# Performance work log

Hardware: AMD Instinct MI355X
Metric: run time of the kernel (lower is better)

Reference implementation:

```python
import jax, jax.numpy as jnp
import numpy as np

VOCAB = 40000
U = 128  # num_trans_units


def setup_inputs() -> dict:
    key = jax.random.key(0)
    ks = jax.random.split(key, 10)
    B, S, T, L = 16, 512, 64, 64
    sents = jax.random.randint(ks[0], (B, S), 0, 30000)
    triples = jax.random.randint(ks[1], (B, T, L, 3), 0, VOCAB)
    sent_triples = jax.random.randint(ks[2], (B, S, 1), 0, T)
    scale = 0.05
    emb_table = jax.random.normal(ks[3], (VOCAB, U), jnp.float32)
    W_trans = jax.random.normal(ks[4], (U, U), jnp.float32) * scale
    b_trans = jnp.zeros((U,), jnp.float32)
    W_ht = jax.random.normal(ks[5], (2 * U, U), jnp.float32) * scale
    b_ht = jnp.zeros((U,), jnp.float32)
    W_rel = jax.random.normal(ks[6], (U, U), jnp.float32) * scale
    b_rel = jnp.zeros((U,), jnp.float32)
    return {
        "sents": sents, "triples": triples, "sent_triples": sent_triples,
        "emb_table": emb_table,
        "W_trans": W_trans, "b_trans": b_trans,
        "W_ht": W_ht, "b_ht": b_ht,
        "W_rel": W_rel, "b_rel": b_rel,
    }


def reference(sents, triples, sent_triples, emb_table,
              W_trans, b_trans, W_ht, b_ht, W_rel, b_rel):
    # triples: [B, T, L, 3] int ids -> embed [B, T, L, 3, U]
    emb = emb_table[triples]
    # fc_trans_transform: Linear(U,U) + Tanh on last dim
    te = jnp.tanh(emb @ W_trans + b_trans)            # [B,T,L,3,U]
    head, relation, tail = te[..., 0, :], te[..., 1, :], te[..., 2, :]
    head_tail = jnp.concatenate([head, tail], axis=-1)  # [B,T,L,2U]
    ht_t = jnp.tanh(head_tail @ W_ht + b_ht)             # [B,T,L,U]
    rel_t = relation @ W_rel + b_rel                     # [B,T,L,U]
    e_weight = jnp.sum(rel_t * ht_t, axis=-1)            # [B,T,L]
    alpha = jax.nn.softmax(e_weight, axis=-1)            # over triple_len L
    graph_embed = jnp.sum(alpha[..., None] * head_tail, axis=2)  # [B,T,2U]
    # gather_nd: out[b, s] = graph_embed[b, sent_triples[b, s, 0]]
    idx = sent_triples[..., 0]                           # [B,S]
    out = jnp.take_along_axis(graph_embed, idx[:, :, None], axis=1)  # [B,S,2U]
    return out
```

## Files before the change

kernel.cpp:

```cpp
#include <hip/hip_runtime.h>
#include <cstdint>
#include <cstddef>

typedef short short8 __attribute__((ext_vector_type(8)));
typedef float f32x4 __attribute__((ext_vector_type(4)));

#define BB 16
#define SS 512
#define TT 64
#define LL 64
#define UU 128

#define WT_OFF    0u
#define WHT_OFF   (WT_OFF + 32768u)
#define WREL_OFF  (WHT_OFF + 65536u)
#define EMBBF_OFF (WREL_OFF + 32768u)
#define EMBBF_BYTES (40000u * 128u * 2u)

__device__ __forceinline__ unsigned short f2bf(float x) {
  unsigned u = __float_as_uint(x);
  unsigned r = ((u >> 16) & 1u) + 0x7FFFu;
  return (unsigned short)((u + r) >> 16);
}
__device__ __forceinline__ float bf2f(unsigned short h) {
  return __uint_as_float(((unsigned)h) << 16);
}
__device__ __forceinline__ float ftanh(float x) {
  float e = __expf(2.0f * x);
  return 1.0f - __fdividef(2.0f, e + 1.0f);
}
__device__ __forceinline__ unsigned cvtpk(float a, float b) {
  unsigned r;
  asm("v_cvt_pk_bf16_f32 %0, %1, %2" : "=v"(r) : "v"(a), "v"(b));
  return r;
}

__global__ void prep_kernel(const float* __restrict__ Wt,
                            const float* __restrict__ Wht,
                            const float* __restrict__ Wrel,
                            const float* __restrict__ ef,
                            unsigned char* __restrict__ ws) {
  int blk = blockIdx.x;
  if (blk < 32) {
    int slot = blk * 256 + threadIdx.x;
    const float* W;
    unsigned char* base;
    if (slot < 2048)      { W = Wt;   base = ws + WT_OFF; }
    else if (slot < 6144) { W = Wht;  base = ws + WHT_OFF;  slot -= 2048; }
    else                  { W = Wrel; base = ws + WREL_OFF; slot -= 6144; }
    int lane = slot & 63, pair = slot >> 6;
    int n  = (pair & 7) * 16 + (lane & 15);
    int k0 = (pair >> 3) * 32 + (lane >> 4) * 8;
    short8 hv;
    #pragma unroll
    for (int j = 0; j < 8; ++j)
      hv[j] = (short)f2bf(W[(size_t)(k0 + j) * UU + n]);
    *reinterpret_cast<short8*>(base + (size_t)pair * 1024 + lane * 16) = hv;
  } else {
    int i = (blk - 32) * 256 + threadIdx.x;
    const float4 a = reinterpret_cast<const float4*>(ef)[i * 2];
    const float4 b = reinterpret_cast<const float4*>(ef)[i * 2 + 1];
    short8 v;
    v[0] = (short)f2bf(a.x); v[1] = (short)f2bf(a.y);
    v[2] = (short)f2bf(a.z); v[3] = (short)f2bf(a.w);
    v[4] = (short)f2bf(b.x); v[5] = (short)f2bf(b.y);
    v[6] = (short)f2bf(b.z); v[7] = (short)f2bf(b.w);
    reinterpret_cast<short8*>(ws + EMBBF_OFF)[i] = v;
  }
}

template<bool PRE>
__launch_bounds__(1024, 8)
__global__ void fused_bt(const int* __restrict__ triples,
                         const float* __restrict__ emb_f32,
                         const unsigned short* __restrict__ emb_bf,
                         const float* __restrict__ b_trans,
                         const float* __restrict__ b_ht,
                         const float* __restrict__ b_rel,
                         const int* __restrict__ sent_triples,
                         const unsigned char* __restrict__ wsr,
                         float* __restrict__ out) {
  __shared__ unsigned short TEB[192 * 128];
  __shared__ float EWt[8][64];
  __shared__ float ALPHA[64];
  __shared__ float PART[4][256];
  int* TOKs = reinterpret_cast<int*>(&PART[0][0]);

  const int tid  = threadIdx.x;
  const int bt   = blockIdx.x;
  const int w    = tid >> 6;
  const int lane = tid & 63;
  const int li   = lane & 15;
  const int lg   = lane >> 4;
  const int nt   = w & 7;
  const int rh   = w >> 3;

  if (tid < 48)
    reinterpret_cast<int4*>(TOKs)[tid] =
        reinterpret_cast<const int4*>(triples + (size_t)bt * 192)[tid];

  const unsigned char* wtb  = wsr + WT_OFF;
  const unsigned char* whtb = wsr + WHT_OFF;
  const unsigned char* wrlb = wsr + WREL_OFF;
  const float bhv   = b_ht[nt * 16 + li];
  const float brlv  = b_rel[nt * 16 + li];
  const float4 btr4 = *reinterpret_cast<const float4*>(b_trans + nt * 16 + lg * 4);
  __syncthreads();

  {
    short8 st[3];
    #pragma unroll
    for (int j = 0; j < 3; ++j) {
      int o = tid + j * 1024;
      int row = o >> 4, pc = o & 15;
      int clog = pc ^ (row & 15);
      if (PRE) {
        st[j] = *reinterpret_cast<const short8*>(
            emb_bf + (size_t)TOKs[row] * UU + clog * 8);
      } else {
        const float* fb = emb_f32 + (size_t)TOKs[row] * UU + clog * 8;
        float4 x = *reinterpret_cast<const float4*>(fb);
        float4 y = *reinterpret_cast<const float4*>(fb + 4);
        st[j][0]=(short)f2bf(x.x); st[j][1]=(short)f2bf(x.y);
        st[j][2]=(short)f2bf(x.z); st[j][3]=(short)f2bf(x.w);
        st[j][4]=(short)f2bf(y.x); st[j][5]=(short)f2bf(y.y);
        st[j][6]=(short)f2bf(y.z); st[j][7]=(short)f2bf(y.w);
      }
    }
    #pragma unroll
    for (int j = 0; j < 3; ++j) {
      int o = tid + j * 1024;
      int row = o >> 4, pc = o & 15;
      *reinterpret_cast<short8*>(&TEB[row * 128 + pc * 8]) = st[j];
    }
  }

  short8 B1h[4];
  #pragma unroll
  for (int kt = 0; kt < 4; ++kt)
    B1h[kt] = *reinterpret_cast<const short8*>(
        wtb + (size_t)(kt * 8 + nt) * 1024 + lane * 16);
  __syncthreads();

  const int cc8 = nt * 2 + (lg >> 1);
  const int hb8 = (lg & 1) << 3;

  f32x4 acc[6];
  #pragma unroll
  for (int q = 0; q < 6; ++q) acc[q] = f32x4{0.f, 0.f, 0.f, 0.f};

  #pragma unroll
  for (int kt = 0; kt < 4; ++kt) {
    #pragma unroll
    for (int q = 0; q < 6; ++q) {
      const short8 b = *reinterpret_cast<const short8*>(
          &TEB[((rh * 6 + q) * 16 + li) * 128 + (((kt * 4 + lg) ^ li) << 3)]);
      acc[q] = __builtin_amdgcn_mfma_f32_16x16x32_bf16(B1h[kt], b, acc[q], 0, 0, 0);
    }
  }
  __syncthreads();

  #pragma unroll
  for (int q = 0; q < 6; ++q) {
    int row = (rh * 6 + q) * 16 + li;
    float v0 = ftanh(acc[q][0] + btr4.x);
    float v1 = ftanh(acc[q][1] + btr4.y);
    float v2 = ftanh(acc[q][2] + btr4.z);
    float v3 = ftanh(acc[q][3] + btr4.w);
    uint2 pk = { cvtpk(v0, v1), cvtpk(v2, v3) };
    *reinterpret_cast<uint2*>(
        reinterpret_cast<char*>(TEB) + row * 256 +
        (((cc8 ^ li) << 4) | hb8)) = pk;
  }

  short8 Wc = *reinterpret_cast<const short8*>(
      whtb + (size_t)nt * 1024 + lane * 16);
  __syncthreads();

  const int mh = rh * 2;
  f32x4 accH[2] = {{0.f,0.f,0.f,0.f},{0.f,0.f,0.f,0.f}};
  f32x4 accR[2] = {{0.f,0.f,0.f,0.f},{0.f,0.f,0.f,0.f}};

  #pragma unroll
  for (int kt = 0; kt < 8; ++kt) {
    short8 Wn;
    if (kt < 7)
      Wn = *reinterpret_cast<const short8*>(
          whtb + (size_t)((kt + 1) * 8 + nt) * 1024 + lane * 16);
    else
      Wn = *reinterpret_cast<const short8*>(
          wrlb + (size_t)nt * 1024 + lane * 16);
    const int koff = (kt < 4) ? 0 : 2;
    const int c16  = (kt & 3) * 4 + lg;
    #pragma unroll
    for (int mi = 0; mi < 2; ++mi) {
      const int row = 48 * (mh + mi) + 3 * li + koff;
      const short8 a = *reinterpret_cast<const short8*>(
          &TEB[row * 128 + ((c16 ^ (row & 15)) << 3)]);
      accH[mi] = __builtin_amdgcn_mfma_f32_16x16x32_bf16(a, Wc, accH[mi], 0, 0, 0);
    }
    Wc = Wn;
  }
  #pragma unroll
  for (int kt = 0; kt < 4; ++kt) {
    short8 Wn;
    if (kt < 3)
      Wn = *reinterpret_cast<const short8*>(
          wrlb + (size_t)((kt + 1) * 8 + nt) * 1024 + lane * 16);
    const int c16 = kt * 4 + lg;
    #pragma unroll
    for (int mi = 0; mi < 2; ++mi) {
      const int row = 48 * (mh + mi) + 3 * li + 1;
      const short8 a = *reinterpret_cast<const short8*>(
          &TEB[row * 128 + ((c16 ^ (row & 15)) << 3)]);
      accR[mi] = __builtin_amdgcn_mfma_f32_16x16x32_bf16(a, Wc, accR[mi], 0, 0, 0);
    }
    Wc = Wn;
  }

  #pragma unroll
  for (int mi = 0; mi < 2; ++mi) {
    #pragma unroll
    for (int r = 0; r < 4; ++r) {
      float p = ftanh(accH[mi][r] + bhv) * (accR[mi][r] + brlv);
      p += __shfl_xor(p, 1, 64);
      p += __shfl_xor(p, 2, 64);
      p += __shfl_xor(p, 4, 64);
      p += __shfl_xor(p, 8, 64);
      if (li == 0) EWt[nt][(mh + mi) * 16 + lg * 4 + r] = p;
    }
  }
  __syncthreads();

  if (tid < 64) {
    float e = 0.f;
    #pragma unroll
    for (int n = 0; n < 8; ++n) e += EWt[n][tid];
    float mx = e;
    #pragma unroll
    for (int off = 32; off > 0; off >>= 1)
      mx = fmaxf(mx, __shfl_xor(mx, off, 64));
    float ex = __expf(e - mx);
    float sm = ex;
    #pragma unroll
    for (int off = 32; off > 0; off >>= 1)
      sm += __shfl_xor(sm, off, 64);
    ALPHA[tid] = ex / sm;
  }
  __syncthreads();

  {
    int c = tid & 255, lgp = tid >> 8;
    int k  = (c >> 7) * 2;
    int cc = c & 127;
    int w8 = cc >> 3, b7 = cc & 7;
    float o = 0.f;
    #pragma unroll
    for (int j = 0; j < 16; ++j) {
      int l = lgp * 16 + j;
      int row = 3 * l + k;
      o = fmaf(ALPHA[l],
               bf2f(TEB[row * 128 + (((w8 ^ (row & 15)) << 3) | b7)]), o);
    }
    PART[lgp][c] = o;
  }
  __syncthreads();

  int* MATCH = reinterpret_cast<int*>(&EWt[0][0]);
  int* NM    = reinterpret_cast<int*>(&ALPHA[0]);
  if (tid < 256)
    PART[0][tid] = PART[0][tid] + PART[1][tid] + PART[2][tid] + PART[3][tid];
  if (tid == 0) *NM = 0;
  __syncthreads();

  {
    int b = bt >> 6, t = bt & 63;
    if (tid < SS) {
      int idx = sent_triples[b * SS + tid];
      if (idx == t) {
        int slot = atomicAdd(NM, 1);
        MATCH[slot] = tid;
      }
    }
    __syncthreads();
    const int nm = *NM;
    const float4 v = reinterpret_cast<const float4*>(&PART[0][0])[lane];
    for (int q = w; q < nm; q += 16) {
      int s = MATCH[q];
      reinterpret_cast<float4*>(out + ((size_t)(b * SS + s)) * 256)[lane] = v;
    }
  }
}

extern "C" void kernel_launch(void* const* d_in, const int* in_sizes, int n_in,
                              void* d_out, int out_size, void* d_ws, size_t ws_size,
                              hipStream_t stream) {
  const int*   triples      = (const int*)d_in[1];
  const int*   sent_triples = (const int*)d_in[2];
  const float* emb_table    = (const float*)d_in[3];
  const float* W_trans      = (const float*)d_in[4];
  const float* b_trans      = (const float*)d_in[5];
  const float* W_ht         = (const float*)d_in[6];
  const float* b_ht         = (const float*)d_in[7];
  const float* W_rel        = (const float*)d_in[8];
  const float* b_rel        = (const float*)d_in[9];
  float* out = (float*)d_out;
  unsigned char* ws = (unsigned char*)d_ws;
  unsigned short* emb_bf = (unsigned short*)(ws + EMBBF_OFF);

  const bool pre = ws_size >= (size_t)EMBBF_OFF + EMBBF_BYTES;

  prep_kernel<<<pre ? 2532 : 32, 256, 0, stream>>>(
      W_trans, W_ht, W_rel, emb_table, ws);

  if (pre)
    fused_bt<true><<<BB * TT, 1024, 0, stream>>>(
        triples, emb_table, emb_bf, b_trans, b_ht, b_rel, sent_triples, ws, out);
  else
    fused_bt<false><<<BB * TT, 1024, 0, stream>>>(
        triples, emb_table, emb_bf, b_trans, b_ht, b_rel, sent_triples, ws, out);
}
```

Before: 50.17 us.

## Rework wave tiling, async gather to LDS, DPP reductions, and hoist match scan

```diff
diff --git a/kernel.cpp b/kernel.cpp
--- a/kernel.cpp
+++ b/kernel.cpp
@@ -17,14 +17,20 @@
 #define EMBBF_OFF (WREL_OFF + 32768u)
 #define EMBBF_BYTES (40000u * 128u * 2u)
 
+#if defined(__has_builtin)
+#  if __has_builtin(__builtin_amdgcn_global_load_lds)
+#    define USE_GLDS 1
+#  endif
+#endif
+#ifndef USE_GLDS
+#  define USE_GLDS 0
+#endif
+
 __device__ __forceinline__ unsigned short f2bf(float x) {
   unsigned u = __float_as_uint(x);
   unsigned r = ((u >> 16) & 1u) + 0x7FFFu;
   return (unsigned short)((u + r) >> 16);
 }
-__device__ __forceinline__ float bf2f(unsigned short h) {
-  return __uint_as_float(((unsigned)h) << 16);
-}
 __device__ __forceinline__ float ftanh(float x) {
   float e = __expf(2.0f * x);
   return 1.0f - __fdividef(2.0f, e + 1.0f);
@@ -34,6 +40,20 @@
   asm("v_cvt_pk_bf16_f32 %0, %1, %2" : "=v"(r) : "v"(a), "v"(b));
   return r;
 }
+__device__ __forceinline__ float row16_sum(float x) {
+  x += __int_as_float(__builtin_amdgcn_update_dpp(0, __float_as_int(x), 0xB1, 0xF, 0xF, true));
+  x += __int_as_float(__builtin_amdgcn_update_dpp(0, __float_as_int(x), 0x4E, 0xF, 0xF, true));
+  x += __int_as_float(__builtin_amdgcn_update_dpp(0, __float_as_int(x), 0x141, 0xF, 0xF, true));
+  x += __int_as_float(__builtin_amdgcn_update_dpp(0, __float_as_int(x), 0x140, 0xF, 0xF, true));
+  return x;
+}
+#if USE_GLDS
+__device__ __forceinline__ void g2lds16(const void* g, void* l) {
+  __builtin_amdgcn_global_load_lds(
+      (const unsigned int __attribute__((address_space(1)))*)g,
+      (unsigned int __attribute__((address_space(3)))*)l, 16, 0, 0);
+}
+#endif
 
 __global__ void prep_kernel(const float* __restrict__ Wt,
                             const float* __restrict__ Wht,
@@ -81,10 +101,11 @@
                          const unsigned char* __restrict__ wsr,
                          float* __restrict__ out) {
   __shared__ unsigned short TEB[192 * 128];
-  __shared__ float EWt[8][64];
+  __shared__ float EWt[4][64];
   __shared__ float ALPHA[64];
-  __shared__ float PART[4][256];
-  int* TOKs = reinterpret_cast<int*>(&PART[0][0]);
+  __shared__ float PART[8][256];
+  __shared__ int MATCH[512];
+  __shared__ int NM;
 
   const int tid  = threadIdx.x;
   const int bt   = blockIdx.x;
@@ -92,150 +113,182 @@
   const int lane = tid & 63;
   const int li   = lane & 15;
   const int lg   = lane >> 4;
-  const int nt   = w & 7;
-  const int rh   = w >> 3;
-
-  if (tid < 48)
-    reinterpret_cast<int4*>(TOKs)[tid] =
-        reinterpret_cast<const int4*>(triples + (size_t)bt * 192)[tid];
+  const int ntp  = w & 3;
+  const int nt0  = ntp * 2, nt1 = nt0 + 1;
+  const int grp  = w >> 2;
 
   const unsigned char* wtb  = wsr + WT_OFF;
   const unsigned char* whtb = wsr + WHT_OFF;
   const unsigned char* wrlb = wsr + WREL_OFF;
-  const float bhv   = b_ht[nt * 16 + li];
-  const float brlv  = b_rel[nt * 16 + li];
-  const float4 btr4 = *reinterpret_cast<const float4*>(b_trans + nt * 16 + lg * 4);
-  __syncthreads();
-
-  {
-    short8 st[3];
+
+  if (tid == 0) NM = 0;
+
+  if (PRE) {
+#if USE_GLDS
     #pragma unroll
     for (int j = 0; j < 3; ++j) {
       int o = tid + j * 1024;
       int row = o >> 4, pc = o & 15;
-      int clog = pc ^ (row & 15);
-      if (PRE) {
-        st[j] = *reinterpret_cast<const short8*>(
-            emb_bf + (size_t)TOKs[row] * UU + clog * 8);
-      } else {
-        const float* fb = emb_f32 + (size_t)TOKs[row] * UU + clog * 8;
-        float4 x = *reinterpret_cast<const float4*>(fb);
-        float4 y = *reinterpret_cast<const float4*>(fb + 4);
-        st[j][0]=(short)f2bf(x.x); st[j][1]=(short)f2bf(x.y);
-        st[j][2]=(short)f2bf(x.z); st[j][3]=(short)f2bf(x.w);
-        st[j][4]=(short)f2bf(y.x); st[j][5]=(short)f2bf(y.y);
-        st[j][6]=(short)f2bf(y.z); st[j][7]=(short)f2bf(y.w);
-      }
+      int tok = triples[(size_t)bt * 192 + row];
+      g2lds16(emb_bf + (size_t)tok * UU + ((pc ^ (row & 15)) << 3),
+              &TEB[o * 8]);
+    }
+#else
+    short8 st[3];
+    #pragma unroll
+    for (int j = 0; j < 3; ++j) {
+      int o = tid + j * 1024, row = o >> 4, pc = o & 15;
+      int tok = triples[(size_t)bt * 192 + row];
+      st[j] = *reinterpret_cast<const short8*>(
+          emb_bf + (size_t)tok * UU + ((pc ^ (row & 15)) << 3));
     }
     #pragma unroll
     for (int j = 0; j < 3; ++j) {
       int o = tid + j * 1024;
-      int row = o >> 4, pc = o & 15;
-      *reinterpret_cast<short8*>(&TEB[row * 128 + pc * 8]) = st[j];
-    }
-  }
-
-  short8 B1h[4];
-  #pragma unroll
-  for (int kt = 0; kt < 4; ++kt)
-    B1h[kt] = *reinterpret_cast<const short8*>(
-        wtb + (size_t)(kt * 8 + nt) * 1024 + lane * 16);
-  __syncthreads();
-
-  const int cc8 = nt * 2 + (lg >> 1);
-  const int hb8 = (lg & 1) << 3;
-
-  f32x4 acc[6];
-  #pragma unroll
-  for (int q = 0; q < 6; ++q) acc[q] = f32x4{0.f, 0.f, 0.f, 0.f};
-
+      *reinterpret_cast<short8*>(&TEB[o * 8]) = st[j];
+    }
+#endif
+  } else {
+    short8 st[3];
+    #pragma unroll
+    for (int j = 0; j < 3; ++j) {
+      int o = tid + j * 1024, row = o >> 4, pc = o & 15;
+      int tok = triples[(size_t)bt * 192 + row];
+      const float* fb = emb_f32 + (size_t)tok * UU + ((pc ^ (row & 15)) << 3);
+      float4 x = *reinterpret_cast<const float4*>(fb);
+      float4 y = *reinterpret_cast<const float4*>(fb + 4);
+      st[j][0]=(short)f2bf(x.x); st[j][1]=(short)f2bf(x.y);
+      st[j][2]=(short)f2bf(x.z); st[j][3]=(short)f2bf(x.w);
+      st[j][4]=(short)f2bf(y.x); st[j][5]=(short)f2bf(y.y);
+      st[j][6]=(short)f2bf(y.z); st[j][7]=(short)f2bf(y.w);
+    }
+    #pragma unroll
+    for (int j = 0; j < 3; ++j) {
+      int o = tid + j * 1024;
+      *reinterpret_cast<short8*>(&TEB[o * 8]) = st[j];
+    }
+  }
+
+  short8 Wa = *reinterpret_cast<const short8*>(wtb + (size_t)nt0 * 1024 + lane * 16);
+  short8 Wb = *reinterpret_cast<const short8*>(wtb + (size_t)nt1 * 1024 + lane * 16);
+  __syncthreads();
+
+  if (tid < SS) {
+    int idx = sent_triples[(bt >> 6) * SS + tid];
+    if (idx == (bt & 63)) MATCH[atomicAdd(&NM, 1)] = tid;
+  }
+
+  f32x4 acc[3][2];
+  #pragma unroll
+  for (int q = 0; q < 3; ++q) {
+    acc[q][0] = f32x4{0.f, 0.f, 0.f, 0.f};
+    acc[q][1] = f32x4{0.f, 0.f, 0.f, 0.f};
+  }
   #pragma unroll
   for (int kt = 0; kt < 4; ++kt) {
-    #pragma unroll
-    for (int q = 0; q < 6; ++q) {
-      const short8 b = *reinterpret_cast<const short8*>(
-          &TEB[((rh * 6 + q) * 16 + li) * 128 + (((kt * 4 + lg) ^ li) << 3)]);
-      acc[q] = __builtin_amdgcn_mfma_f32_16x16x32_bf16(B1h[kt], b, acc[q], 0, 0, 0);
-    }
-  }
-  __syncthreads();
-
-  #pragma unroll
-  for (int q = 0; q < 6; ++q) {
-    int row = (rh * 6 + q) * 16 + li;
-    float v0 = ftanh(acc[q][0] + btr4.x);
-    float v1 = ftanh(acc[q][1] + btr4.y);
-    float v2 = ftanh(acc[q][2] + btr4.z);
-    float v3 = ftanh(acc[q][3] + btr4.w);
-    uint2 pk = { cvtpk(v0, v1), cvtpk(v2, v3) };
-    *reinterpret_cast<uint2*>(
-        reinterpret_cast<char*>(TEB) + row * 256 +
-        (((cc8 ^ li) << 4) | hb8)) = pk;
-  }
-
-  short8 Wc = *reinterpret_cast<const short8*>(
-      whtb + (size_t)nt * 1024 + lane * 16);
-  __syncthreads();
-
-  const int mh = rh * 2;
-  f32x4 accH[2] = {{0.f,0.f,0.f,0.f},{0.f,0.f,0.f,0.f}};
-  f32x4 accR[2] = {{0.f,0.f,0.f,0.f},{0.f,0.f,0.f,0.f}};
+    if (kt > 0) {
+      Wa = *reinterpret_cast<const short8*>(
+          wtb + (size_t)(kt * 8 + nt0) * 1024 + lane * 16);
+      Wb = *reinterpret_cast<const short8*>(
+          wtb + (size_t)(kt * 8 + nt1) * 1024 + lane * 16);
+    }
+    #pragma unroll
+    for (int q = 0; q < 3; ++q) {
+      const short8 bfr = *reinterpret_cast<const short8*>(
+          &TEB[((grp * 3 + q) * 16 + li) * 128 + (((kt * 4 + lg) ^ li) << 3)]);
+      acc[q][0] = __builtin_amdgcn_mfma_f32_16x16x32_bf16(Wa, bfr, acc[q][0], 0, 0, 0);
+      acc[q][1] = __builtin_amdgcn_mfma_f32_16x16x32_bf16(Wb, bfr, acc[q][1], 0, 0, 0);
+    }
+  }
+  __syncthreads();
+
+  const float4 btrA = *reinterpret_cast<const float4*>(b_trans + nt0 * 16 + lg * 4);
+  const float4 btrB = *reinterpret_cast<const float4*>(b_trans + nt1 * 16 + lg * 4);
+  const int hb8  = (lg & 1) << 3;
+  const int cc8A = nt0 * 2 + (lg >> 1);
+  const int cc8B = cc8A + 2;
+  #pragma unroll
+  for (int q = 0; q < 3; ++q) {
+    int row = (grp * 3 + q) * 16 + li;
+    char* base = reinterpret_cast<char*>(TEB) + row * 256;
+    {
+      float v0 = ftanh(acc[q][0][0] + btrA.x);
+      float v1 = ftanh(acc[q][0][1] + btrA.y);
+      float v2 = ftanh(acc[q][0][2] + btrA.z);
+      float v3 = ftanh(acc[q][0][3] + btrA.w);
+      uint2 pk = { cvtpk(v0, v1), cvtpk(v2, v3) };
+      *reinterpret_cast<uint2*>(base + (((cc8A ^ li) << 4) | hb8)) = pk;
+    }
+    {
+      float v0 = ftanh(acc[q][1][0] + btrB.x);
+      float v1 = ftanh(acc[q][1][1] + btrB.y);
+      float v2 = ftanh(acc[q][1][2] + btrB.z);
+      float v3 = ftanh(acc[q][1][3] + btrB.w);
+      uint2 pk = { cvtpk(v0, v1), cvtpk(v2, v3) };
+      *reinterpret_cast<uint2*>(base + (((cc8B ^ li) << 4) | hb8)) = pk;
+    }
+  }
+
+  short8 Wc0 = *reinterpret_cast<const short8*>(whtb + (size_t)nt0 * 1024 + lane * 16);
+  short8 Wc1 = *reinterpret_cast<const short8*>(whtb + (size_t)nt1 * 1024 + lane * 16);
+  __syncthreads();
+
+  const int m    = grp;
+  const int rowb = 48 * m + 3 * li;
+  const float bh0 = b_ht[nt0 * 16 + li],  bh1 = b_ht[nt1 * 16 + li];
+  const float br0 = b_rel[nt0 * 16 + li], br1 = b_rel[nt1 * 16 + li];
+  f32x4 aH0{0.f,0.f,0.f,0.f}, aH1{0.f,0.f,0.f,0.f};
+  f32x4 aR0{0.f,0.f,0.f,0.f}, aR1{0.f,0.f,0.f,0.f};
 
   #pragma unroll
   for (int kt = 0; kt < 8; ++kt) {
-    short8 Wn;
-    if (kt < 7)
-      Wn = *reinterpret_cast<const short8*>(
-          whtb + (size_t)((kt + 1) * 8 + nt) * 1024 + lane * 16);
-    else
-      Wn = *reinterpret_cast<const short8*>(
-          wrlb + (size_t)nt * 1024 + lane * 16);
-    const int koff = (kt < 4) ? 0 : 2;
-    const int c16  = (kt & 3) * 4 + lg;
-    #pragma unroll
-    for (int mi = 0; mi < 2; ++mi) {
-      const int row = 48 * (mh + mi) + 3 * li + koff;
-      const short8 a = *reinterpret_cast<const short8*>(
-          &TEB[row * 128 + ((c16 ^ (row & 15)) << 3)]);
-      accH[mi] = __builtin_amdgcn_mfma_f32_16x16x32_bf16(a, Wc, accH[mi], 0, 0, 0);
-    }
-    Wc = Wn;
+    short8 Wn0, Wn1;
+    if (kt < 7) {
+      Wn0 = *reinterpret_cast<const short8*>(
+          whtb + (size_t)((kt + 1) * 8 + nt0) * 1024 + lane * 16);
+      Wn1 = *reinterpret_cast<const short8*>(
+          whtb + (size_t)((kt + 1) * 8 + nt1) * 1024 + lane * 16);
+    } else {
+      Wn0 = *reinterpret_cast<const short8*>(wrlb + (size_t)nt0 * 1024 + lane * 16);
+      Wn1 = *reinterpret_cast<const short8*>(wrlb + (size_t)nt1 * 1024 + lane * 16);
+    }
+    const int row = rowb + ((kt < 4) ? 0 : 2);
+    const int c16 = (kt & 3) * 4 + lg;
+    const short8 a = *reinterpret_cast<const short8*>(
+        &TEB[row * 128 + ((c16 ^ (row & 15)) << 3)]);
+    aH0 = __builtin_amdgcn_mfma_f32_16x16x32_bf16(a, Wc0, aH0, 0, 0, 0);
+    aH1 = __builtin_amdgcn_mfma_f32_16x16x32_bf16(a, Wc1, aH1, 0, 0, 0);
+    Wc0 = Wn0; Wc1 = Wn1;
   }
   #pragma unroll
   for (int kt = 0; kt < 4; ++kt) {
-    short8 Wn;
-    if (kt < 3)
-      Wn = *reinterpret_cast<const short8*>(
-          wrlb + (size_t)((kt + 1) * 8 + nt) * 1024 + lane * 16);
+    short8 Wn0, Wn1;
+    if (kt < 3) {
+      Wn0 = *reinterpret_cast<const short8*>(
+          wrlb + (size_t)((kt + 1) * 8 + nt0) * 1024 + lane * 16);
+      Wn1 = *reinterpret_cast<const short8*>(
+          wrlb + (size_t)((kt + 1) * 8 + nt1) * 1024 + lane * 16);
+    }
+    const int row = rowb + 1;
     const int c16 = kt * 4 + lg;
-    #pragma unroll
-    for (int mi = 0; mi < 2; ++mi) {
-      const int row = 48 * (mh + mi) + 3 * li + 1;
-      const short8 a = *reinterpret_cast<const short8*>(
-          &TEB[row * 128 + ((c16 ^ (row & 15)) << 3)]);
-      accR[mi] = __builtin_amdgcn_mfma_f32_16x16x32_bf16(a, Wc, accR[mi], 0, 0, 0);
-    }
-    Wc = Wn;
-  }
-
-  #pragma unroll
-  for (int mi = 0; mi < 2; ++mi) {
-    #pragma unroll
-    for (int r = 0; r < 4; ++r) {
-      float p = ftanh(accH[mi][r] + bhv) * (accR[mi][r] + brlv);
-      p += __shfl_xor(p, 1, 64);
-      p += __shfl_xor(p, 2, 64);
-      p += __shfl_xor(p, 4, 64);
-      p += __shfl_xor(p, 8, 64);
-      if (li == 0) EWt[nt][(mh + mi) * 16 + lg * 4 + r] = p;
-    }
+    const short8 a = *reinterpret_cast<const short8*>(
+        &TEB[row * 128 + ((c16 ^ (row & 15)) << 3)]);
+    aR0 = __builtin_amdgcn_mfma_f32_16x16x32_bf16(a, Wc0, aR0, 0, 0, 0);
+    aR1 = __builtin_amdgcn_mfma_f32_16x16x32_bf16(a, Wc1, aR1, 0, 0, 0);
+    if (kt < 3) { Wc0 = Wn0; Wc1 = Wn1; }
+  }
+
+  #pragma unroll
+  for (int r = 0; r < 4; ++r) {
+    float p = ftanh(aH0[r] + bh0) * (aR0[r] + br0)
+            + ftanh(aH1[r] + bh1) * (aR1[r] + br1);
+    p = row16_sum(p);
+    if (li == 0) EWt[ntp][m * 16 + lg * 4 + r] = p;
   }
   __syncthreads();
 
   if (tid < 64) {
-    float e = 0.f;
-    #pragma unroll
-    for (int n = 0; n < 8; ++n) e += EWt[n][tid];
+    float e = EWt[0][tid] + EWt[1][tid] + EWt[2][tid] + EWt[3][tid];
     float mx = e;
     #pragma unroll
     for (int off = 32; off > 0; off >>= 1)
@@ -250,40 +303,40 @@
   __syncthreads();
 
   {
-    int c = tid & 255, lgp = tid >> 8;
-    int k  = (c >> 7) * 2;
-    int cc = c & 127;
-    int w8 = cc >> 3, b7 = cc & 7;
-    float o = 0.f;
-    #pragma unroll
-    for (int j = 0; j < 16; ++j) {
-      int l = lgp * 16 + j;
+    int cp  = tid & 127, lgp = tid >> 7;
+    int c0  = cp << 1;
+    int k   = (c0 >> 7) << 1;
+    int cc  = c0 & 127;
+    int w8  = cc >> 3, bofs = (cc & 7) << 1;
+    float4 a03 = *reinterpret_cast<const float4*>(&ALPHA[lgp * 8]);
+    float4 a47 = *reinterpret_cast<const float4*>(&ALPHA[lgp * 8 + 4]);
+    float o0 = 0.f, o1 = 0.f;
+    #pragma unroll
+    for (int j = 0; j < 8; ++j) {
+      int l = lgp * 8 + j;
       int row = 3 * l + k;
-      o = fmaf(ALPHA[l],
-               bf2f(TEB[row * 128 + (((w8 ^ (row & 15)) << 3) | b7)]), o);
-    }
-    PART[lgp][c] = o;
-  }
-  __syncthreads();
-
-  int* MATCH = reinterpret_cast<int*>(&EWt[0][0]);
-  int* NM    = reinterpret_cast<int*>(&ALPHA[0]);
-  if (tid < 256)
-    PART[0][tid] = PART[0][tid] + PART[1][tid] + PART[2][tid] + PART[3][tid];
-  if (tid == 0) *NM = 0;
+      unsigned u = *reinterpret_cast<const unsigned*>(
+          reinterpret_cast<const char*>(TEB) + row * 256 +
+          (((w8 ^ (row & 15)) << 4) | bofs));
+      float al = (j < 4) ? a03[j] : a47[j - 4];
+      o0 = fmaf(al, __uint_as_float(u << 16), o0);
+      o1 = fmaf(al, __uint_as_float(u & 0xFFFF0000u), o1);
+    }
+    *reinterpret_cast<float2*>(&PART[lgp][c0]) = make_float2(o0, o1);
+  }
+  __syncthreads();
+
+  if (tid < 256) {
+    float s = 0.f;
+    #pragma unroll
+    for (int g = 0; g < 8; ++g) s += PART[g][tid];
+    PART[0][tid] = s;
+  }
   __syncthreads();
 
   {
-    int b = bt >> 6, t = bt & 63;
-    if (tid < SS) {
-      int idx = sent_triples[b * SS + tid];
-      if (idx == t) {
-        int slot = atomicAdd(NM, 1);
-        MATCH[slot] = tid;
-      }
-    }
-    __syncthreads();
-    const int nm = *NM;
+    int b = bt >> 6;
+    const int nm = NM;
     const float4 v = reinterpret_cast<const float4*>(&PART[0][0])[lane];
     for (int q = w; q < nm; q += 16) {
       int s = MATCH[q];
```

New measurement: 51.13 us. No clear change (+1.9%).

## Drop full embedding bf16 pre-conversion; convert gathered rows in-kernel with packed cvt

Applied to the files above, without the earlier changes.

```diff
diff --git a/kernel.cpp b/kernel.cpp
--- a/kernel.cpp
+++ b/kernel.cpp
@@ -14,8 +14,6 @@
 #define WT_OFF    0u
 #define WHT_OFF   (WT_OFF + 32768u)
 #define WREL_OFF  (WHT_OFF + 65536u)
-#define EMBBF_OFF (WREL_OFF + 32768u)
-#define EMBBF_BYTES (40000u * 128u * 2u)
 
 __device__ __forceinline__ unsigned short f2bf(float x) {
   unsigned u = __float_as_uint(x);
@@ -34,46 +32,37 @@
   asm("v_cvt_pk_bf16_f32 %0, %1, %2" : "=v"(r) : "v"(a), "v"(b));
   return r;
 }
+__device__ __forceinline__ float row16_sum(float x) {
+  x += __int_as_float(__builtin_amdgcn_update_dpp(0, __float_as_int(x), 0xB1, 0xF, 0xF, true));
+  x += __int_as_float(__builtin_amdgcn_update_dpp(0, __float_as_int(x), 0x4E, 0xF, 0xF, true));
+  x += __int_as_float(__builtin_amdgcn_update_dpp(0, __float_as_int(x), 0x141, 0xF, 0xF, true));
+  x += __int_as_float(__builtin_amdgcn_update_dpp(0, __float_as_int(x), 0x140, 0xF, 0xF, true));
+  return x;
+}
 
 __global__ void prep_kernel(const float* __restrict__ Wt,
                             const float* __restrict__ Wht,
                             const float* __restrict__ Wrel,
-                            const float* __restrict__ ef,
                             unsigned char* __restrict__ ws) {
-  int blk = blockIdx.x;
-  if (blk < 32) {
-    int slot = blk * 256 + threadIdx.x;
-    const float* W;
-    unsigned char* base;
-    if (slot < 2048)      { W = Wt;   base = ws + WT_OFF; }
-    else if (slot < 6144) { W = Wht;  base = ws + WHT_OFF;  slot -= 2048; }
-    else                  { W = Wrel; base = ws + WREL_OFF; slot -= 6144; }
-    int lane = slot & 63, pair = slot >> 6;
-    int n  = (pair & 7) * 16 + (lane & 15);
-    int k0 = (pair >> 3) * 32 + (lane >> 4) * 8;
-    short8 hv;
-    #pragma unroll
-    for (int j = 0; j < 8; ++j)
-      hv[j] = (short)f2bf(W[(size_t)(k0 + j) * UU + n]);
-    *reinterpret_cast<short8*>(base + (size_t)pair * 1024 + lane * 16) = hv;
-  } else {
-    int i = (blk - 32) * 256 + threadIdx.x;
-    const float4 a = reinterpret_cast<const float4*>(ef)[i * 2];
-    const float4 b = reinterpret_cast<const float4*>(ef)[i * 2 + 1];
-    short8 v;
-    v[0] = (short)f2bf(a.x); v[1] = (short)f2bf(a.y);
-    v[2] = (short)f2bf(a.z); v[3] = (short)f2bf(a.w);
-    v[4] = (short)f2bf(b.x); v[5] = (short)f2bf(b.y);
-    v[6] = (short)f2bf(b.z); v[7] = (short)f2bf(b.w);
-    reinterpret_cast<short8*>(ws + EMBBF_OFF)[i] = v;
-  }
-}
-
-template<bool PRE>
+  int slot = blockIdx.x * 256 + threadIdx.x;
+  const float* W;
+  unsigned char* base;
+  if (slot < 2048)      { W = Wt;   base = ws + WT_OFF; }
+  else if (slot < 6144) { W = Wht;  base = ws + WHT_OFF;  slot -= 2048; }
+  else                  { W = Wrel; base = ws + WREL_OFF; slot -= 6144; }
+  int lane = slot & 63, pair = slot >> 6;
+  int n  = (pair & 7) * 16 + (lane & 15);
+  int k0 = (pair >> 3) * 32 + (lane >> 4) * 8;
+  short8 hv;
+  #pragma unroll
+  for (int j = 0; j < 8; ++j)
+    hv[j] = (short)f2bf(W[(size_t)(k0 + j) * UU + n]);
+  *reinterpret_cast<short8*>(base + (size_t)pair * 1024 + lane * 16) = hv;
+}
+
 __launch_bounds__(1024, 8)
 __global__ void fused_bt(const int* __restrict__ triples,
                          const float* __restrict__ emb_f32,
-                         const unsigned short* __restrict__ emb_bf,
                          const float* __restrict__ b_trans,
                          const float* __restrict__ b_ht,
                          const float* __restrict__ b_rel,
@@ -83,7 +72,7 @@
   __shared__ unsigned short TEB[192 * 128];
   __shared__ float EWt[8][64];
   __shared__ float ALPHA[64];
-  __shared__ float PART[4][256];
+  __shared__ float PART[8][256];
   int* TOKs = reinterpret_cast<int*>(&PART[0][0]);
 
   const int tid  = threadIdx.x;
@@ -95,6 +84,9 @@
   const int nt   = w & 7;
   const int rh   = w >> 3;
 
+  int sidx = 0;
+  if (tid < SS) sidx = sent_triples[(size_t)(bt >> 6) * SS + tid];
+
   if (tid < 48)
     reinterpret_cast<int4*>(TOKs)[tid] =
         reinterpret_cast<const int4*>(triples + (size_t)bt * 192)[tid];
@@ -108,30 +100,22 @@
   __syncthreads();
 
   {
-    short8 st[3];
+    float4 xv[3], yv[3];
     #pragma unroll
     for (int j = 0; j < 3; ++j) {
       int o = tid + j * 1024;
       int row = o >> 4, pc = o & 15;
       int clog = pc ^ (row & 15);
-      if (PRE) {
-        st[j] = *reinterpret_cast<const short8*>(
-            emb_bf + (size_t)TOKs[row] * UU + clog * 8);
-      } else {
-        const float* fb = emb_f32 + (size_t)TOKs[row] * UU + clog * 8;
-        float4 x = *reinterpret_cast<const float4*>(fb);
-        float4 y = *reinterpret_cast<const float4*>(fb + 4);
-        st[j][0]=(short)f2bf(x.x); st[j][1]=(short)f2bf(x.y);
-        st[j][2]=(short)f2bf(x.z); st[j][3]=(short)f2bf(x.w);
-        st[j][4]=(short)f2bf(y.x); st[j][5]=(short)f2bf(y.y);
-        st[j][6]=(short)f2bf(y.z); st[j][7]=(short)f2bf(y.w);
-      }
+      const float* fb = emb_f32 + (size_t)TOKs[row] * UU + clog * 8;
+      xv[j] = *reinterpret_cast<const float4*>(fb);
+      yv[j] = *reinterpret_cast<const float4*>(fb + 4);
     }
     #pragma unroll
     for (int j = 0; j < 3; ++j) {
       int o = tid + j * 1024;
-      int row = o >> 4, pc = o & 15;
-      *reinterpret_cast<short8*>(&TEB[row * 128 + pc * 8]) = st[j];
+      uint4 pk = { cvtpk(xv[j].x, xv[j].y), cvtpk(xv[j].z, xv[j].w),
+                   cvtpk(yv[j].x, yv[j].y), cvtpk(yv[j].z, yv[j].w) };
+      *reinterpret_cast<uint4*>(&TEB[o * 8]) = pk;
     }
   }
 
@@ -223,10 +207,7 @@
     #pragma unroll
     for (int r = 0; r < 4; ++r) {
       float p = ftanh(accH[mi][r] + bhv) * (accR[mi][r] + brlv);
-      p += __shfl_xor(p, 1, 64);
-      p += __shfl_xor(p, 2, 64);
-      p += __shfl_xor(p, 4, 64);
-      p += __shfl_xor(p, 8, 64);
+      p = row16_sum(p);
       if (li == 0) EWt[nt][(mh + mi) * 16 + lg * 4 + r] = p;
     }
   }
@@ -250,37 +231,45 @@
   __syncthreads();
 
   {
-    int c = tid & 255, lgp = tid >> 8;
-    int k  = (c >> 7) * 2;
-    int cc = c & 127;
-    int w8 = cc >> 3, b7 = cc & 7;
-    float o = 0.f;
-    #pragma unroll
-    for (int j = 0; j < 16; ++j) {
-      int l = lgp * 16 + j;
+    int cp  = tid & 127, lgp = tid >> 7;
+    int c0  = cp << 1;
+    int k   = (c0 >> 7) << 1;
+    int cc  = c0 & 127;
+    int w8  = cc >> 3, bofs = (cc & 7) << 1;
+    float4 a03 = *reinterpret_cast<const float4*>(&ALPHA[lgp * 8]);
+    float4 a47 = *reinterpret_cast<const float4*>(&ALPHA[lgp * 8 + 4]);
+    float o0 = 0.f, o1 = 0.f;
+    #pragma unroll
+    for (int j = 0; j < 8; ++j) {
+      int l = lgp * 8 + j;
       int row = 3 * l + k;
-      o = fmaf(ALPHA[l],
-               bf2f(TEB[row * 128 + (((w8 ^ (row & 15)) << 3) | b7)]), o);
-    }
-    PART[lgp][c] = o;
+      unsigned u = *reinterpret_cast<const unsigned*>(
+          reinterpret_cast<const char*>(TEB) + row * 256 +
+          (((w8 ^ (row & 15)) << 4) | bofs));
+      float al = (j < 4) ? a03[j] : a47[j - 4];
+      o0 = fmaf(al, __uint_as_float(u << 16), o0);
+      o1 = fmaf(al, __uint_as_float(u & 0xFFFF0000u), o1);
+    }
+    *reinterpret_cast<float2*>(&PART[lgp][c0]) = make_float2(o0, o1);
   }
   __syncthreads();
 
   int* MATCH = reinterpret_cast<int*>(&EWt[0][0]);
   int* NM    = reinterpret_cast<int*>(&ALPHA[0]);
-  if (tid < 256)
-    PART[0][tid] = PART[0][tid] + PART[1][tid] + PART[2][tid] + PART[3][tid];
+  if (tid < 256) {
+    float s = 0.f;
+    #pragma unroll
+    for (int g = 0; g < 8; ++g) s += PART[g][tid];
+    PART[0][tid] = s;
+  }
   if (tid == 0) *NM = 0;
   __syncthreads();
 
   {
     int b = bt >> 6, t = bt & 63;
-    if (tid < SS) {
-      int idx = sent_triples[b * SS + tid];
-      if (idx == t) {
-        int slot = atomicAdd(NM, 1);
-        MATCH[slot] = tid;
-      }
+    if (tid < SS && sidx == t) {
+      int slot = atomicAdd(NM, 1);
+      MATCH[slot] = tid;
     }
     __syncthreads();
     const int nm = *NM;
@@ -306,17 +295,9 @@
   const float* b_rel        = (const float*)d_in[9];
   float* out = (float*)d_out;
   unsigned char* ws = (unsigned char*)d_ws;
-  unsigned short* emb_bf = (unsigned short*)(ws + EMBBF_OFF);
-
-  const bool pre = ws_size >= (size_t)EMBBF_OFF + EMBBF_BYTES;
-
-  prep_kernel<<<pre ? 2532 : 32, 256, 0, stream>>>(
-      W_trans, W_ht, W_rel, emb_table, ws);
-
-  if (pre)
-    fused_bt<true><<<BB * TT, 1024, 0, stream>>>(
-        triples, emb_table, emb_bf, b_trans, b_ht, b_rel, sent_triples, ws, out);
-  else
-    fused_bt<false><<<BB * TT, 1024, 0, stream>>>(
-        triples, emb_table, emb_bf, b_trans, b_ht, b_rel, sent_triples, ws, out);
-}
+
+  prep_kernel<<<32, 256, 0, stream>>>(W_trans, W_ht, W_rel, ws);
+
+  fused_bt<<<BB * TT, 1024, 0, stream>>>(
+      triples, emb_table, b_trans, b_ht, b_rel, sent_triples, ws, out);
+}
```

Result: faster. 47.34 us (-5.6%).
